# Optimization experiments

Measured on AMD Instinct MI355X. Metric: run time of the kernel, lower is better.

Reference implementation:

```python
import jax, jax.numpy as jnp
import numpy as np

N, IN, HID, OUT, HD = 512, 256, 256, 256, 64  # n_agents, in_dim, hid_dim, out_dim, head_dim (out_dim // n_heads)


def _mlp2(x, w1, b1, w2, b2):
    return jax.nn.relu(x @ w1.T + b1) @ w2.T + b2


def setup_inputs():
    key = jax.random.key(0)
    ks = jax.random.split(key, 32)
    p = lambda i, shape: jax.random.normal(ks[i], shape, dtype=jnp.float32) * 0.05
    V = jax.random.normal(ks[0], (N, IN), dtype=jnp.float32)
    adj = jax.random.randint(ks[1], (N, N), 0, 2, dtype=jnp.int32)
    adj = adj.at[jnp.arange(N), jnp.arange(N)].set(1)  # self-loops so no softmax row is all -inf
    prev_hidden = jax.random.normal(ks[2], (N, HID), dtype=jnp.float32)
    return {
        "V": V, "adj": adj, "prev_hidden": prev_hidden,
        "W1": p(3, (HID, IN)), "sa0": p(4, (HID,)), "sa1": p(5, (HID,)),
        "ce_w1": p(6, (HID, 2 * IN)), "ce_b1": p(7, (HID,)), "ce_w2": p(8, (HD, HID)), "ce_b2": p(9, (HD,)),
        "ca0": p(10, (HD,)), "ca1": p(11, (HD,)),
        "te_w1": p(12, (HID, IN + HID)), "te_b1": p(13, (HID,)), "te_w2": p(14, (HD, HID)), "te_b2": p(15, (HD,)),
        "ta0": p(16, (HD,)), "ta1": p(17, (HD,)),
        "pe_w1": p(18, (HID, 3 * IN)), "pe_b1": p(19, (HID,)), "pe_w2": p(20, (HD, HID)), "pe_b2": p(21, (HD,)),
        "pa0": p(22, (HD,)), "pa1": p(23, (HD,)),
        "W2": p(24, (OUT, HID + 2 * HD + 1)), "op_w": p(25, (OUT, OUT)), "op_b": p(26, (OUT,)),
        "ln_g": jnp.ones((OUT,), jnp.float32), "ln_b": jnp.zeros((OUT,), jnp.float32),
    }


def _forward(V, adj, prev_hidden, W1, sa0, sa1, ce_w1, ce_b1, ce_w2, ce_b2, ca0, ca1,
             te_w1, te_b1, te_w2, te_b2, ta0, ta1, pe_w1, pe_b1, pe_w2, pe_b2, pa0, pa1,
             W2, op_w, op_b, ln_g, ln_b):
    neg = -jnp.inf
    # --- branch 1: standard GAT attention ---
    Wh1 = V @ W1.T                                             # (N, HID)
    s1 = (Wh1 @ sa0)[:, None] + (Wh1 @ sa1)[None, :]           # (N, N)
    s1 = jnp.where(adj == 0, neg, s1)
    H1 = jax.nn.softmax(s1, axis=1) @ Wh1                      # (N, HID)
    # --- branch 2: causal, all ordered pairs i != j ---
    wA, wB = ce_w1[:, :IN], ce_w1[:, IN:]
    h = jax.nn.relu((V @ wA.T)[:, None, :] + (V @ wB.T)[None, :, :] + ce_b1)  # (N, N, HID)
    f = h @ ce_w2.T + ce_b2                                    # (N, N, HD)
    s2 = jnp.where(jnp.eye(N, dtype=bool), neg, f @ (ca0 + ca1))
    a2 = jax.nn.softmax(s2.reshape(-1)).reshape(N, N)          # softmax over all off-diagonal pairs
    H2 = jnp.broadcast_to(jnp.einsum('ij,ijd->d', a2, f), (N, HD))
    # --- branch 3: temporal; (N,1) scores broadcast against (N,N) causal mask ---
    tf = _mlp2(jnp.concatenate([V, prev_hidden], -1), te_w1, te_b1, te_w2, te_b2)  # (N, HD)
    ts = tf @ (ta0 + ta1)                                      # (N,)
    cmask = jnp.triu(jnp.ones((N, N), dtype=bool), 1)
    s3 = jnp.where(cmask, neg, jnp.broadcast_to(ts[:, None], (N, N)))
    H3 = jax.nn.softmax(s3, axis=1) @ tf                       # (N, HD) == prefix means of tf
    # --- branch 4: cooperative; first two neighbors in index order (zeros if < 2) ---
    pos = jnp.where(adj == 1, jnp.arange(N)[None, :], N)
    srt = jnp.sort(pos, axis=1)
    i0, i1 = srt[:, 0], srt[:, 1]
    valid = (i1 < N)[:, None]
    n0 = jnp.where(valid, V[jnp.clip(i0, 0, N - 1)], 0.0)
    n1 = jnp.where(valid, V[jnp.clip(i1, 0, N - 1)], 0.0)
    cf = _mlp2(jnp.concatenate([V, n0, n1], -1), pe_w1, pe_b1, pe_w2, pe_b2)  # (N, HD)
    # torch: softmax over dim of size 1 -> all ones, alpha^T @ cf == column sums -> (HD,)
    # then unsqueezed to (HD,1) and zero-padded to (N,1) since HD < N  (faithful to source bug)
    H4v = cf.sum(axis=0)
    H4 = jnp.concatenate([H4v, jnp.zeros((N - HD,), V.dtype)])[:, None]       # (N, 1)
    # --- combine ---
    Hc = jnp.concatenate([H1, H2, H3, H4], axis=-1) @ W2.T     # (N, OUT)
    out = Hc @ op_w.T + op_b
    mu = out.mean(-1, keepdims=True)
    var = ((out - mu) ** 2).mean(-1, keepdims=True)
    y = (out - mu) / jnp.sqrt(var + 1e-5) * ln_g + ln_b        # LayerNorm, eps=1e-5
    return jax.nn.elu(y)                                       # dropout is identity in eval


def reference(V, adj, prev_hidden, W1, sa0, sa1, ce_w1, ce_b1, ce_w2, ce_b2, ca0, ca1,
              te_w1, te_b1, te_w2, te_b2, ta0, ta1, pe_w1, pe_b1, pe_w2, pe_b2, pa0, pa1,
              W2, op_w, op_b, ln_g, ln_b):
    return _forward(V, adj, prev_hidden, W1, sa0, sa1, ce_w1, ce_b1, ce_w2, ce_b2, ca0, ca1,
                    te_w1, te_b1, te_w2, te_b2, ta0, ta1, pe_w1, pe_b1, pe_w2, pe_b2, pa0, pa1,
                    W2, op_w, op_b, ln_g, ln_b)
```

## Files before the change

### kernel.cpp

```cpp
#include <hip/hip_runtime.h>

typedef unsigned short u16;

constexpr int kN   = 512;
constexpr int kIN  = 256;
constexpr int kHID = 256;
constexpr int kHD  = 64;
constexpr int kOUT = 256;

__device__ __forceinline__ float us2f(u16 u){
  union { unsigned int i; float f; } c; c.i = ((unsigned int)u) << 16; return c.f;
}
__device__ __forceinline__ u16 f2us(float f){
  union { float f; unsigned int i; } c; c.f = f;
  unsigned int r = c.i + 0x7fff + ((c.i >> 16) & 1);
  return (u16)(r >> 16);
}
__device__ __forceinline__ float ldraw(const void* p, size_t i, bool f32){
  return f32 ? ((const float*)p)[i] : us2f(((const u16*)p)[i]);
}

__device__ bool probe_is_f32(const unsigned int* __restrict__ V){
  __shared__ int cnt;
  if (threadIdx.x == 0) cnt = 0;
  __syncthreads();
  int c = 0;
  for (int k = threadIdx.x; k < 4096; k += 256){
    float x = us2f((u16)(V[k] & 0xffffu));
    if (!(fabsf(x) <= 32.0f)) c++;
  }
  atomicAdd(&cnt, c);
  __syncthreads();
  return cnt > 64;
}

__device__ __forceinline__ float blk_red(float v, float* tmp, bool isMax){
  int lane = threadIdx.x & 63, wv = threadIdx.x >> 6;
  #pragma unroll
  for (int o = 32; o > 0; o >>= 1){
    float t = __shfl_down(v, o, 64);
    v = isMax ? fmaxf(v, t) : (v + t);
  }
  __syncthreads();
  if (lane == 0) tmp[wv] = v;
  __syncthreads();
  float r = tmp[0];
  for (int i = 1; i < 4; ++i) r = isMax ? fmaxf(r, tmp[i]) : (r + tmp[i]);
  return r;
}

constexpr int kNConv = 23;
struct ConvArgs { const void* src[kNConv]; float* dst[kNConv]; int n[kNConv]; };
struct GSeg2 { const float* X; const float* W; float* C; int ldx, ldw, ldc, K; };
struct GS32 { const float* X; const float* W; float* C; int ldx, ldw, ldc, K; int bkn; };

struct Args {
  const unsigned int* Vraw;
  const int* adj;
  int* flag; void* out;
  const void *rca0,*rca1,*rcw2,*rcb2,*rtw2,*rpw2;
  float *Vf,*prevf,*W1f,*sa1f,*cw1f,*cb1f,*cw2f,*cb2f,*ca0f,*ca1f;
  float *tw1f,*tb1f,*tw2f,*tb2f,*pw1f,*pb1f,*pw2f,*pb2f;
  float *W2f,*opwf,*opbf,*lngf,*lnbf;
  float *tw2t,*pw2t,*Wcomb,*OM,*ow4;
  float *Wh1,*e1v,*wadj,*Hc,*Am,*Bm,*uvec,*beta;
  float *s2,*maxp,*zp,*MZ,*gsum;
  float *htp0,*htp1,*hpp0,*hpp1,*hpp2,*hidden_t,*hidden_p;
  float *tfm,*cfm,*H4v,*Xp,*out3;
  ConvArgs ca;
  GSeg2 gs[8];
};

__device__ __forceinline__ void gemm32_body(const GS32 sg, int tm, int tn, int tid,
                                            float* Xs, float* Ws)
{
  const int i0 = tm << 5, n0 = tn << 5;
  const int xrow = tid >> 3;
  const int xk = (tid & 7) << 2;
  const int rg = (tid >> 4) << 1;
  const int cg = (tid & 15) << 1;
  const float* Xb = sg.X + (size_t)i0 * sg.ldx;
  const float* Wb = sg.bkn ? (sg.W + n0) : (sg.W + (size_t)n0 * sg.ldw);
  float4 xr, wr;
  auto loadT = [&](int kt){
    xr = *(const float4*)(Xb + (size_t)xrow * sg.ldx + kt + xk);
    if (sg.bkn) wr = *(const float4*)(Wb + (size_t)(kt + xrow) * sg.ldw + xk);
    else        wr = *(const float4*)(Wb + (size_t)xrow * sg.ldw + kt + xk);
  };
  auto writeT = [&](int bu){
    float* xs = Xs + bu*1152;
    xs[(xk+0)*36 + xrow] = xr.x; xs[(xk+1)*36 + xrow] = xr.y;
    xs[(xk+2)*36 + xrow] = xr.z; xs[(xk+3)*36 + xrow] = xr.w;
    float* wsp = Ws + bu*1152;
    if (sg.bkn){
      wsp[xrow*36 + xk+0] = wr.x; wsp[xrow*36 + xk+1] = wr.y;
      wsp[xrow*36 + xk+2] = wr.z; wsp[xrow*36 + xk+3] = wr.w;
    } else {
      wsp[(xk+0)*36 + xrow] = wr.x; wsp[(xk+1)*36 + xrow] = wr.y;
      wsp[(xk+2)*36 + xrow] = wr.z; wsp[(xk+3)*36 + xrow] = wr.w;
    }
  };
  loadT(0); writeT(0); __syncthreads();
  float a00=0,a01=0,a10=0,a11=0;
  const int nkt = sg.K >> 5;
  for (int t = 0; t < nkt; ++t){
    if (t+1 < nkt) loadT((t+1) << 5);
    const float* xs = Xs + (t&1)*1152;
    const float* wsp = Ws + (t&1)*1152;
    #pragma unroll
    for (int kk = 0; kk < 32; ++kk){
      float2 av = *(const float2*)&xs[kk*36 + rg];
      float2 bv = *(const float2*)&wsp[kk*36 + cg];
      a00 += av.x*bv.x; a01 += av.x*bv.y;
      a10 += av.y*bv.x; a11 += av.y*bv.y;
    }
    if (t+1 < nkt) writeT((t+1)&1);
    __syncthreads();
  }
  float* cp = sg.C + (size_t)(i0+rg)*sg.ldc + n0 + cg;
  *(float2*)cp = make_float2(a00, a01);
  *(float2*)(cp + sg.ldc) = make_float2(a10, a11);
}

__device__ void body_gemmA(const Args& A, int it, int tid, char* SM)
{
  float (*Xs)[32][68] = (float (*)[32][68])SM;
  float (*Ws)[32][68] = (float (*)[32][68])(SM + 17408);
  int seg = it >> 5, x = it & 31;
  const GSeg2 sg = A.gs[seg];
  const int tm = x & 7, tn = x >> 3;
  const int i0 = tm << 6, n0 = tn << 6;

  const int xrow = tid >> 3;
  const int xk   = (tid & 7) << 2;
  const int rg = (tid >> 4) << 2;
  const int cg = (tid & 15) << 2;

  const float* Xb = sg.X + (size_t)i0 * sg.ldx;
  const float* Wb = sg.W + (size_t)n0 * sg.ldw;

  float4 xr0, xr1, wr0, wr1;
  auto loadT = [&](int kt){
    xr0 = *(const float4*)(Xb + (size_t)xrow * sg.ldx + kt + xk);
    xr1 = *(const float4*)(Xb + (size_t)(xrow+32) * sg.ldx + kt + xk);
    wr0 = *(const float4*)(Wb + (size_t)xrow * sg.ldw + kt + xk);
    wr1 = *(const float4*)(Wb + (size_t)(xrow+32) * sg.ldw + kt + xk);
  };
  auto writeT = [&](int bu){
    Xs[bu][xk+0][xrow] = xr0.x;  Xs[bu][xk+1][xrow] = xr0.y;
    Xs[bu][xk+2][xrow] = xr0.z;  Xs[bu][xk+3][xrow] = xr0.w;
    Xs[bu][xk+0][xrow+32] = xr1.x;  Xs[bu][xk+1][xrow+32] = xr1.y;
    Xs[bu][xk+2][xrow+32] = xr1.z;  Xs[bu][xk+3][xrow+32] = xr1.w;
    Ws[bu][xk+0][xrow]    = wr0.x; Ws[bu][xk+1][xrow]    = wr0.y;
    Ws[bu][xk+2][xrow]    = wr0.z; Ws[bu][xk+3][xrow]    = wr0.w;
    Ws[bu][xk+0][xrow+32] = wr1.x; Ws[bu][xk+1][xrow+32] = wr1.y;
    Ws[bu][xk+2][xrow+32] = wr1.z; Ws[bu][xk+3][xrow+32] = wr1.w;
  };

  loadT(0); writeT(0); __syncthreads();

  float acc[4][4] = {};
  const int nkt = sg.K >> 5;
  for (int t = 0; t < nkt; ++t){
    if (t + 1 < nkt) loadT((t + 1) << 5);
    const int bu = t & 1;
    #pragma unroll
    for (int kk = 0; kk < 32; ++kk){
      const float4 av = *(const float4*)&Xs[bu][kk][rg];
      const float4 bv = *(const float4*)&Ws[bu][kk][cg];
      acc[0][0]+=av.x*bv.x; acc[0][1]+=av.x*bv.y; acc[0][2]+=av.x*bv.z; acc[0][3]+=av.x*bv.w;
      acc[1][0]+=av.y*bv.x; acc[1][1]+=av.y*bv.y; acc[1][2]+=av.y*bv.z; acc[1][3]+=av.y*bv.w;
      acc[2][0]+=av.z*bv.x; acc[2][1]+=av.z*bv.y; acc[2][2]+=av.z*bv.z; acc[2][3]+=av.z*bv.w;
      acc[3][0]+=av.w*bv.x; acc[3][1]+=av.w*bv.y; acc[3][2]+=av.w*bv.z; acc[3][3]+=av.w*bv.w;
    }
    if (t + 1 < nkt) writeT((t + 1) & 1);
    __syncthreads();
  }

  #pragma unroll
  for (int ri = 0; ri < 4; ++ri)
    *(float4*)(sg.C + (size_t)(i0 + rg + ri) * sg.ldc + (n0 + cg)) =
      make_float4(acc[ri][0], acc[ri][1], acc[ri][2], acc[ri][3]);

  if (seg == 0){
    int cb = n0 + cg;
    float s0 = A.sa1f[cb], s1 = A.sa1f[cb+1], s2v = A.sa1f[cb+2], s3 = A.sa1f[cb+3];
    #pragma unroll
    for (int ri = 0; ri < 4; ++ri){
      float v = acc[ri][0]*s0 + acc[ri][1]*s1 + acc[ri][2]*s2v + acc[ri][3]*s3;
      v += __shfl_xor(v, 1, 16);
      v += __shfl_xor(v, 2, 16);
      v += __shfl_xor(v, 4, 16);
      v += __shfl_xor(v, 8, 16);
      if ((tid & 15) == 0) atomicAdd(&A.e1v[i0 + rg + ri], v);
    }
  }
}

__global__ __launch_bounds__(256) void k_s0(Args A)
{
  __shared__ __align__(16) char SM[16896];
  int it = blockIdx.x, tid = threadIdx.x;
  bool f32 = probe_is_f32(A.Vraw);
  if (it < 256){
    if (it == 0){
      if (tid == 0) *A.flag = f32 ? 1 : 0;
      A.e1v[tid] = 0.f; A.e1v[tid + 256] = 0.f;
    }
    int t = it*256 + tid;
    for (int s = 0; s < kNConv; ++s){
      int n4 = A.ca.n[s] >> 2;
      float4* d = (float4*)A.ca.dst[s];
      if (f32){
        const float4* sf = (const float4*)A.ca.src[s];
        for (int i = t; i < n4; i += 65536) d[i] = sf[i];
      } else {
        const ushort4* sb = (const ushort4*)A.ca.src[s];
        for (int i = t; i < n4; i += 65536){
          ushort4 u = sb[i];
          d[i] = make_float4(us2f(u.x), us2f(u.y), us2f(u.z), us2f(u.w));
        }
      }
    }
  } else if (it < 768){
    unsigned long long* msk = (unsigned long long*)SM;
    int* sj = (int*)(SM + 64);
    int i = it - 256;
    int w = tid >> 6, lane = tid & 63;
    unsigned long long m0 = __ballot(A.adj[(size_t)i*kN + tid] != 0);
    unsigned long long m1 = __ballot(A.adj[(size_t)i*kN + 256 + tid] != 0);
    if (lane == 0){ msk[w] = m0; msk[4 + w] = m1; }
    __syncthreads();
    if (tid == 0){
      int j0 = -1, j1 = -1;
      for (int c = 0; c < 8 && j1 < 0; ++c){
        unsigned long long m = msk[c];
        while (m && j1 < 0){
          int bb = __builtin_ctzll(m);
          int j = c*64 + bb;
          if (j0 < 0) j0 = j; else j1 = j;
          m &= m - 1;
        }
      }
      if (j1 < 0) j0 = -1;
      sj[0] = j0; sj[1] = j1;
    }
    __syncthreads();
    int j0 = sj[0], j1 = sj[1];
    A.Xp[(size_t)i*768 + tid]       = ldraw(A.Vraw, (size_t)i*kIN + tid, f32);
    A.Xp[(size_t)i*768 + 256 + tid] = (j0 >= 0) ? ldraw(A.Vraw, (size_t)j0*kIN + tid, f32) : 0.f;
    A.Xp[(size_t)i*768 + 512 + tid] = (j1 >= 0) ? ldraw(A.Vraw, (size_t)j1*kIN + tid, f32) : 0.f;
  } else if (it == 768){
    float* st = (float*)SM;
    if (tid < 64){ st[tid] = ldraw(A.rca0, tid, f32) + ldraw(A.rca1, tid, f32); A.H4v[tid] = 0.f; }
    __syncthreads();
    float a = 0.f;
    for (int d = 0; d < kHD; ++d) a += ldraw(A.rcw2, (size_t)d*kHID + tid, f32) * st[d];
    A.uvec[tid] = a;
    if (tid == 0){
      float b = 0.f;
      for (int d = 0; d < kHD; ++d) b += ldraw(A.rcb2, d, f32) * st[d];
      *A.beta = b;
    }
  } else {
    const void* src = (it == 769) ? A.rtw2 : A.rpw2;
    float* dst = (it == 769) ? A.tw2t : A.pw2t;
    float* st = (float*)SM;
    for (int ch = 0; ch < 4; ++ch){
      __syncthreads();
      #pragma unroll
      for (int e = 0; e < 16; ++e){
        int lin = e*256 + tid, r = lin >> 6, c = lin & 63;
        st[r*65 + c] = ldraw(src, (size_t)r*256 + ch*64 + c, f32);
      }
      __syncthreads();
      #pragma unroll
      for (int e = 0; e < 16; ++e){
        int lin = e*256 + tid, kc = lin >> 6, dd = lin & 63;
        dst[(size_t)(ch*64 + kc)*64 + dd] = st[dd*65 + kc];
      }
    }
  }
}

__global__ __launch_bounds__(256) void k_s1(Args A)
{
  __shared__ __align__(16) char SM[34816];
  int it = blockIdx.x, tid = threadIdx.x;
  if (it < 256){
    body_gemmA(A, it, tid, SM);
  } else if (it < 336){
    int q = it - 256, tm = q & 7, tn = q >> 3;
    const float* Wsrc = A.W2f + ((tn < 8) ? 0 : 64);
    GS32 sg{A.opwf, Wsrc, A.Wcomb, 256, 385, 320, 256, 1};
    gemm32_body(sg, tm, tn, tid, (float*)SM, (float*)(SM + 9216));
  } else if (it < 352){
    int q = it - 336;
    GS32 sg{A.opwf, A.W2f + 256, A.OM, 256, 385, 64, 256, 1};
    gemm32_body(sg, q & 7, q >> 3, tid, (float*)SM, (float*)(SM + 9216));
  } else {
    float* st = (float*)SM;
    st[tid] = A.W2f[(size_t)tid*385 + 384];
    __syncthreads();
    float a = 0.f;
    const float* orow = A.opwf + (size_t)tid*256;
    for (int m = 0; m < 256; m += 4){
      float4 o4 = *(const float4*)(orow + m);
      a += o4.x*st[m] + o4.y*st[m+1] + o4.z*st[m+2] + o4.w*st[m+3];
    }
    A.ow4[tid] = a;
  }
}

__global__ __launch_bounds__(256) void k_s2(Args A)
{
  __shared__ float SM2[8];
  int it = blockIdx.x, tid = threadIdx.x;
  if (it < 128){
    int f = it*256 + tid;
    int c4 = f & 63;
    {
      float4 a = ((const float4*)A.htp0)[f], bb = ((const float4*)A.htp1)[f];
      float4 bi = ((const float4*)A.tb1f)[c4];
      ((float4*)A.hidden_t)[f] = make_float4(
        fmaxf(a.x+bb.x+bi.x,0.f), fmaxf(a.y+bb.y+bi.y,0.f),
        fmaxf(a.z+bb.z+bi.z,0.f), fmaxf(a.w+bb.w+bi.w,0.f));
    }
    {
      float4 a = ((const float4*)A.hpp0)[f], bb = ((const float4*)A.hpp1)[f];
      float4 c = ((const float4*)A.hpp2)[f];
      float4 bi = ((const float4*)A.pb1f)[c4];
      ((float4*)A.hidden_p)[f] = make_float4(
        fmaxf(a.x+bb.x+c.x+bi.x,0.f), fmaxf(a.y+bb.y+c.y+bi.y,0.f),
        fmaxf(a.z+bb.z+c.z+bi.z,0.f), fmaxf(a.w+bb.w+c.w+bi.w,0.f));
    }
  } else {
    int i = it - 128;
    int m0 = A.adj[(size_t)i*kN + tid];
    int m1 = A.adj[(size_t)i*kN + tid + 256];
    float ea = A.e1v[tid], eb = A.e1v[tid+256];
    float v0 = m0 ? ea : -1e30f;
    float v1 = m1 ? eb : -1e30f;
    float m = blk_red(fmaxf(v0, v1), SM2, true);
    float z = blk_red((m0 ? expf(ea-m) : 0.f) + (m1 ? expf(eb-m) : 0.f), SM2, false);
    float iz = 1.0f / z;
    A.wadj[(size_t)i*kN + tid]       = m0 ? expf(ea - m) * iz : 0.f;
    A.wadj[(size_t)i*kN + tid + 256] = m1 ? expf(eb - m) * iz : 0.f;
  }
}

__global__ __launch_bounds__(256) void k_s3(Args A)
{
  __shared__ __align__(16) float SM3[32*36*2 + 256 + 256 + 8];
  int it = blockIdx.x, tid = threadIdx.x;
  if (it < 64){
    int m = it >> 5, grp = it & 31;
    const float* X  = m ? A.hidden_p : A.hidden_t;
    const float* Wt = m ? A.pw2t : A.tw2t;
    const float* bi = m ? A.pb2f : A.tb2f;
    float* C = m ? A.cfm : A.tfm;
    int i0 = grp*16 + (tid >> 6)*4;
    int d = tid & 63;
    const float* x0 = X + (size_t)i0*256;
    const float* x1 = x0 + 256;
    const float* x2 = x0 + 512;
    const float* x3 = x0 + 768;
    float a0=0.f, a1=0.f, a2=0.f, a3=0.f;
    for (int k = 0; k < 256; k += 4){
      float w0 = Wt[(size_t)(k+0)*64 + d];
      float w1 = Wt[(size_t)(k+1)*64 + d];
      float w2 = Wt[(size_t)(k+2)*64 + d];
      float w3 = Wt[(size_t)(k+3)*64 + d];
      float4 f0 = *(const float4*)(x0 + k);
      float4 f1 = *(const float4*)(x1 + k);
      float4 f2 = *(const float4*)(x2 + k);
      float4 f3 = *(const float4*)(x3 + k);
      a0 += f0.x*w0 + f0.y*w1 + f0.z*w2 + f0.w*w3;
      a1 += f1.x*w0 + f1.y*w1 + f1.z*w2 + f1.w*w3;
      a2 += f2.x*w0 + f2.y*w1 + f2.z*w2 + f2.w*w3;
      a3 += f3.x*w0 + f3.y*w1 + f3.z*w2 + f3.w*w3;
    }
    float bd = bi[d];
    C[(size_t)(i0+0)*64 + d] = a0 + bd;
    C[(size_t)(i0+1)*64 + d] = a1 + bd;
    C[(size_t)(i0+2)*64 + d] = a2 + bd;
    C[(size_t)(i0+3)*64 + d] = a3 + bd;
  } else {
    float* As = SM3;
    float* Bs = As + 32*36;
    float* Us = Bs + 32*36;
    float* B1 = Us + 256;
    float* red = B1 + 256;
    int q = it - 64;
    int i0 = (q & 15) * 32, j0 = (q >> 4) * 32;
    Us[tid] = A.uvec[tid];
    B1[tid] = A.cb1f[tid];
    const int xrow = tid >> 3;
    const int xk   = (tid & 7) << 2;
    const int rg = (tid >> 4) << 1;
    const int cg = (tid & 15) << 1;
    float acc[2][2] = {};
    for (int kt = 0; kt < 256; kt += 32){
      __syncthreads();
      float4 av = *(const float4*)(A.Am + (size_t)(i0+xrow)*kHID + kt + xk);
      float4 bv = *(const float4*)(A.Bm + (size_t)(j0+xrow)*kHID + kt + xk);
      As[(xk+0)*36 + xrow] = av.x + B1[kt+xk+0];
      As[(xk+1)*36 + xrow] = av.y + B1[kt+xk+1];
      As[(xk+2)*36 + xrow] = av.z + B1[kt+xk+2];
      As[(xk+3)*36 + xrow] = av.w + B1[kt+xk+3];
      Bs[(xk+0)*36 + xrow] = bv.x;
      Bs[(xk+1)*36 + xrow] = bv.y;
      Bs[(xk+2)*36 + xrow] = bv.z;
      Bs[(xk+3)*36 + xrow] = bv.w;
      __syncthreads();
      #pragma unroll
      for (int kk = 0; kk < 32; ++kk){
        float uk = Us[kt + kk];
        float2 a2 = *(const float2*)&As[kk*36 + rg];
        float2 b2 = *(const float2*)&Bs[kk*36 + cg];
        acc[0][0] += fmaxf(a2.x + b2.x, 0.f) * uk;
        acc[0][1] += fmaxf(a2.x + b2.y, 0.f) * uk;
        acc[1][0] += fmaxf(a2.y + b2.x, 0.f) * uk;
        acc[1][1] += fmaxf(a2.y + b2.y, 0.f) * uk;
      }
    }
    float bet = *A.beta;
    float sv[2][2];
    #pragma unroll
    for (int r = 0; r < 2; ++r){
      #pragma unroll
      for (int c = 0; c < 2; ++c){
        float vsc = acc[r][c] + bet;
        int i = i0 + rg + r, j = j0 + cg + c;
        if (i == j) vsc = -1e30f;
        sv[r][c] = vsc;
        A.s2[(size_t)i*kN + j] = vsc;
      }
    }
    __syncthreads();
    float m = blk_red(fmaxf(fmaxf(sv[0][0], sv[0][1]), fmaxf(sv[1][0], sv[1][1])), red, true);
    float z = expf(sv[0][0]-m) + expf(sv[0][1]-m) + expf(sv[1][0]-m) + expf(sv[1][1]-m);
    z = blk_red(z, red, false);
    if (tid == 0){ A.maxp[q] = m; A.zp[q] = z; }
  }
}

__global__ __launch_bounds__(256) void k_s4(Args A)
{
  __shared__ __align__(16) char SM[18432];
  int it = blockIdx.x, tid = threadIdx.x;
  if (it < 128){
    GS32 sg{A.wadj, A.Wh1, A.Hc, 512, 256, 320, 512, 1};
    gemm32_body(sg, it & 15, it >> 4, tid, (float*)SM, (float*)(SM + 9216));
  } else if (it < 192){
    int d = it - 128;
    int lane = tid & 63, wv = tid >> 6;
    float v0 = A.tfm[(size_t)(2*tid)*kHD + d];
    float v1 = A.tfm[(size_t)(2*tid+1)*kHD + d];
    float s = v0 + v1;
    float x = s;
    #pragma unroll
    for (int off = 1; off < 64; off <<= 1){
      float y = __shfl_up(x, off, 64);
      if (lane >= off) x += y;
    }
    float* wsum = (float*)SM;
    if (lane == 63) wsum[wv] = x;
    __syncthreads();
    float base = 0.f;
    for (int k = 0; k < wv; ++k) base += wsum[k];
    float excl = base + x - s;
    A.Hc[(size_t)(2*tid)*320 + 256 + d]   = (excl + v0) / (float)(2*tid + 1);
    A.Hc[(size_t)(2*tid+1)*320 + 256 + d] = (excl + s)  / (float)(2*tid + 2);
  } else if (it < 200){
    float* sm = (float*)SM;
    int d = tid & 63, sub = tid >> 6;
    int r0 = (it-192)*64 + sub*16;
    float s = 0.f;
    #pragma unroll
    for (int e = 0; e < 16; ++e) s += A.cfm[(size_t)(r0+e)*kHD + d];
    sm[sub*64 + d] = s;
    __syncthreads();
    if (tid < 64)
      atomicAdd(&A.H4v[tid], sm[tid] + sm[64+tid] + sm[128+tid] + sm[192+tid]);
  } else {
    float* red = (float*)SM;
    float m = blk_red(A.maxp[tid], red, true);
    float z = A.zp[tid] * expf(A.maxp[tid] - m);
    z = blk_red(z, red, false);
    if (tid == 0){ A.MZ[0] = m; A.MZ[1] = z; }
    A.gsum[tid] = 0.f;
  }
}

__global__ __launch_bounds__(256) void k_s5(Args A)
{
  __shared__ __align__(16) char SM[18432];
  int it = blockIdx.x, tid = threadIdx.x;
  if (it < 1024){
    float* wt = (float*)SM;
    int i0 = (it & 31) * 16, j0 = (it >> 5) * 16;
    float M = A.MZ[0], invZ = 1.0f / A.MZ[1];
    {
      int r = tid >> 4, c = tid & 15;
      wt[r*16 + c] = expf(A.s2[(size_t)(i0+r)*kN + (j0+c)] - M) * invZ;
    }
    float b1v = A.cb1f[tid];
    float aib[16];
    #pragma unroll
    for (int r = 0; r < 16; ++r) aib[r] = A.Am[(size_t)(i0+r)*kHID + tid] + b1v;
    __syncthreads();
    float acc = 0.f;
    for (int j = 0; j < 16; ++j){
      float bj = A.Bm[(size_t)(j0+j)*kHID + tid];
      #pragma unroll
      for (int r = 0; r < 16; ++r)
        acc += wt[r*16 + j] * fmaxf(aib[r] + bj, 0.f);
    }
    atomicAdd(&A.gsum[tid], acc);
  } else {
    int q = it - 1024;
    GS32 sg{A.Hc, A.Wcomb, A.out3, 320, 320, 256, 320, 0};
    gemm32_body(sg, q & 15, q >> 4, tid, (float*)SM, (float*)(SM + 9216));
  }
}

__global__ __launch_bounds__(256) void k_s6(Args A)
{
  __shared__ float gs[kHID];
  __shared__ float part[kHD][4];
  __shared__ float h2s[kHD];
  __shared__ float cc2s[kOUT];
  int b = blockIdx.x, tid = threadIdx.x;
  bool f32 = (*A.flag != 0);
  gs[tid] = A.gsum[tid];
  __syncthreads();
  {
    int dd = tid >> 2, q = tid & 3;
    float a = 0.f;
    for (int kk = 0; kk < 64; ++kk){
      int k = q*64 + kk;
      a += gs[k] * A.cw2f[(size_t)dd*kHID + k];
    }
    part[dd][q] = a;
  }
  __syncthreads();
  if (tid < kHD)
    h2s[tid] = A.cb2f[tid] + part[tid][0] + part[tid][1] + part[tid][2] + part[tid][3];
  __syncthreads();
  {
    float a = 0.f;
    const float* om = A.OM + (size_t)tid*64;
    for (int d = 0; d < kHD; d += 4){
      float4 o4 = *(const float4*)(om + d);
      a += o4.x*h2s[d] + o4.y*h2s[d+1] + o4.z*h2s[d+2] + o4.w*h2s[d+3];
    }
    cc2s[tid] = a;
  }
  __syncthreads();
  int row = b*4 + (tid >> 6), lane = tid & 63;
  float h4r = (row < kHD) ? A.H4v[row] : 0.f;
  float4 v  = *(const float4*)(A.out3 + (size_t)row*kOUT + lane*4);
  float4 c2 = *(const float4*)(&cc2s[lane*4]);
  float4 o4 = *(const float4*)(A.ow4 + lane*4);
  float4 pb = *(const float4*)(A.opbf + lane*4);
  v.x += c2.x + h4r*o4.x + pb.x;
  v.y += c2.y + h4r*o4.y + pb.y;
  v.z += c2.z + h4r*o4.z + pb.z;
  v.w += c2.w + h4r*o4.w + pb.w;
  float s = v.x + v.y + v.z + v.w;
  #pragma unroll
  for (int o = 32; o > 0; o >>= 1) s += __shfl_xor(s, o, 64);
  float mu = s * (1.0f/kOUT);
  float dx = v.x-mu, dy = v.y-mu, dz = v.z-mu, dw = v.w-mu;
  float ss = dx*dx + dy*dy + dz*dz + dw*dw;
  #pragma unroll
  for (int o = 32; o > 0; o >>= 1) ss += __shfl_xor(ss, o, 64);
  float rs = rsqrtf(ss * (1.0f/kOUT) + 1e-5f);
  float4 g  = *(const float4*)(A.lngf + lane*4);
  float4 be = *(const float4*)(A.lnbf + lane*4);
  float y0 = dx*rs*g.x + be.x, y1 = dy*rs*g.y + be.y;
  float y2 = dz*rs*g.z + be.z, y3 = dw*rs*g.w + be.w;
  y0 = (y0 > 0.f) ? y0 : expm1f(y0);
  y1 = (y1 > 0.f) ? y1 : expm1f(y1);
  y2 = (y2 > 0.f) ? y2 : expm1f(y2);
  y3 = (y3 > 0.f) ? y3 : expm1f(y3);
  if (f32){
    *(float4*)((float*)A.out + (size_t)row*kOUT + lane*4) = make_float4(y0,y1,y2,y3);
  } else {
    ushort4 u; u.x = f2us(y0); u.y = f2us(y1); u.z = f2us(y2); u.w = f2us(y3);
    ((ushort4*)A.out)[(size_t)row*64 + lane] = u;
  }
}

extern "C" void kernel_launch(void* const* d_in, const int* in_sizes, int n_in,
                              void* d_out, int out_size, void* d_ws, size_t ws_size,
                              hipStream_t stream)
{
  const void* V     = d_in[0];
  const int*  adj   = (const int*)d_in[1];
  const void* prev  = d_in[2];
  const void* W1    = d_in[3];
  const void* sa1   = d_in[5];
  const void* ce_w1 = d_in[6];
  const void* ce_b1 = d_in[7];
  const void* ce_w2 = d_in[8];
  const void* ce_b2 = d_in[9];
  const void* ca0   = d_in[10];
  const void* ca1   = d_in[11];
  const void* te_w1 = d_in[12];
  const void* te_b1 = d_in[13];
  const void* te_w2 = d_in[14];
  const void* te_b2 = d_in[15];
  const void* pe_w1 = d_in[18];
  const void* pe_b1 = d_in[19];
  const void* pe_w2 = d_in[20];
  const void* pe_b2 = d_in[21];
  const void* W2    = d_in[24];
  const void* op_w  = d_in[25];
  const void* op_b  = d_in[26];
  const void* ln_g  = d_in[27];
  const void* ln_b  = d_in[28];

  float* ws  = (float*)d_ws;
  int*  flag = (int*)ws;
  float* p   = ws + 16;
  float* Vf   = p; p += 131072;
  float* prevf= p; p += 131072;
  float* W1f  = p; p += 65536;
  float* sa1f = p; p += 256;
  float* cw1f = p; p += 131072;
  float* cb1f = p; p += 256;
  float* cw2f = p; p += 16384;
  float* cb2f = p; p += 64;
  float* ca0f = p; p += 64;
  float* ca1f = p; p += 64;
  float* tw1f = p; p += 131072;
  float* tb1f = p; p += 256;
  float* tw2f = p; p += 16384;
  float* tb2f = p; p += 64;
  float* pw1f = p; p += 196608;
  float* pb1f = p; p += 256;
  float* pw2f = p; p += 16384;
  float* pb2f = p; p += 64;
  float* W2f  = p; p += 98560;
  float* opwf = p; p += 65536;
  float* opbf = p; p += 256;
  float* lngf = p; p += 256;
  float* lnbf = p; p += 256;
  float* tw2t = p; p += 16384;
  float* pw2t = p; p += 16384;
  float* Wcomb= p; p += 81920;
  float* OM   = p; p += 16384;
  float* ow4  = p; p += 256;
  float* Wh1      = p; p += 131072;
  float* e1v      = p; p += 512;
  float* wadj     = p; p += 262144;
  float* Hc       = p; p += 163840;
  float* Am       = p; p += 131072;
  float* Bm       = p; p += 131072;
  float* uvec     = p; p += 256;
  float* beta     = p; p += 16;
  float* s2       = p; p += 262144;
  float* maxp     = p; p += 4096;
  float* zpart    = p; p += 4096;
  float* MZ       = p; p += 16;
  float* gsum     = p; p += 256;
  float* htp0     = p; p += 131072;
  float* htp1     = p; p += 131072;
  float* hpp0     = p; p += 131072;
  float* hpp1     = p; p += 131072;
  float* hpp2     = p; p += 131072;
  float* hidden_t = p; p += 131072;
  float* hidden_p = p; p += 131072;
  float* tfm      = p; p += 32768;
  float* cfm      = p; p += 32768;
  float* H4v      = p; p += 64;
  float* Xp       = p; p += 393216;
  float* out3     = p; p += 131072;

  Args A;
  A.Vraw = (const unsigned int*)V; A.adj = adj;
  A.flag = flag; A.out = d_out;
  A.rca0 = ca0; A.rca1 = ca1; A.rcw2 = ce_w2; A.rcb2 = ce_b2; A.rtw2 = te_w2; A.rpw2 = pe_w2;
  A.Vf=Vf; A.prevf=prevf; A.W1f=W1f; A.sa1f=sa1f; A.cw1f=cw1f; A.cb1f=cb1f;
  A.cw2f=cw2f; A.cb2f=cb2f; A.ca0f=ca0f; A.ca1f=ca1f;
  A.tw1f=tw1f; A.tb1f=tb1f; A.tw2f=tw2f; A.tb2f=tb2f;
  A.pw1f=pw1f; A.pb1f=pb1f; A.pw2f=pw2f; A.pb2f=pb2f;
  A.W2f=W2f; A.opwf=opwf; A.opbf=opbf; A.lngf=lngf; A.lnbf=lnbf;
  A.tw2t=tw2t; A.pw2t=pw2t; A.Wcomb=Wcomb; A.OM=OM; A.ow4=ow4;
  A.Wh1=Wh1; A.e1v=e1v; A.wadj=wadj; A.Hc=Hc;
  A.Am=Am; A.Bm=Bm; A.uvec=uvec; A.beta=beta;
  A.s2=s2; A.maxp=maxp; A.zp=zpart; A.MZ=MZ; A.gsum=gsum;
  A.htp0=htp0; A.htp1=htp1; A.hpp0=hpp0; A.hpp1=hpp1; A.hpp2=hpp2;
  A.hidden_t=hidden_t; A.hidden_p=hidden_p;
  A.tfm=tfm; A.cfm=cfm; A.H4v=H4v; A.Xp=Xp; A.out3=out3;

  {
    const void* srcs[kNConv] = {V, prev, W1, sa1, ce_w1, ce_b1, ce_w2, ce_b2, ca0, ca1,
                                te_w1, te_b1, te_w2, te_b2, pe_w1, pe_b1, pe_w2, pe_b2,
                                W2, op_w, op_b, ln_g, ln_b};
    float* dsts[kNConv] = {Vf, prevf, W1f, sa1f, cw1f, cb1f, cw2f, cb2f, ca0f, ca1f,
                           tw1f, tb1f, tw2f, tb2f, pw1f, pb1f, pw2f, pb2f,
                           W2f, opwf, opbf, lngf, lnbf};
    int ns[kNConv] = {131072, 131072, 65536, 256, 131072, 256, 16384, 64, 64, 64,
                      131072, 256, 16384, 64, 196608, 256, 16384, 64,
                      98560, 65536, 256, 256, 256};
    for (int s = 0; s < kNConv; ++s){ A.ca.src[s] = srcs[s]; A.ca.dst[s] = dsts[s]; A.ca.n[s] = ns[s]; }
  }
  A.gs[0] = {Vf,       W1f,        Wh1,  256, 256, 256, 256};
  A.gs[1] = {Vf,       cw1f,       Am,   256, 512, 256, 256};
  A.gs[2] = {Vf,       cw1f + 256, Bm,   256, 512, 256, 256};
  A.gs[3] = {Vf,       tw1f,       htp0, 256, 512, 256, 256};
  A.gs[4] = {prevf,    tw1f + 256, htp1, 256, 512, 256, 256};
  A.gs[5] = {Xp,       pw1f,       hpp0, 768, 768, 256, 256};
  A.gs[6] = {Xp + 256, pw1f + 256, hpp1, 768, 768, 256, 256};
  A.gs[7] = {Xp + 512, pw1f + 512, hpp2, 768, 768, 256, 256};

  k_s0<<<771,  256, 0, stream>>>(A);
  k_s1<<<353,  256, 0, stream>>>(A);
  k_s2<<<640,  256, 0, stream>>>(A);
  k_s3<<<320,  256, 0, stream>>>(A);
  k_s4<<<201,  256, 0, stream>>>(A);
  k_s5<<<1152, 256, 0, stream>>>(A);
  k_s6<<<128,  256, 0, stream>>>(A);
}
```

Before: 235.5 us.

## Fuse causal softmax-weighted accumulation into score kernel with per-block max rescale

Each 32x32 score tile now computes its local max and exponentials and immediately accumulates the weighted relu hidden sum into a per-block partial vector. A later reduction rescales these partials by exp(local max minus global max) and divides by the global normalizer. This removes the N×N score buffer round trip, the 1024-block atomicAdd pass and one kernel launch. The hidden_t/hidden_p relu+bias elementwise pass is folded into the downstream GEMV loads, and the final GEMM moves into its own kernel. In exchange the score blocks do more per-block work, partial sums are summed in a different order, and the GEMV reads two or three partial buffers instead of one.

```diff
diff --git a/kernel.cpp b/kernel.cpp
--- a/kernel.cpp
+++ b/kernel.cpp
@@ -64,8 +64,8 @@
   float *W2f,*opwf,*opbf,*lngf,*lnbf;
   float *tw2t,*pw2t,*Wcomb,*OM,*ow4;
   float *Wh1,*e1v,*wadj,*Hc,*Am,*Bm,*uvec,*beta;
-  float *s2,*maxp,*zp,*MZ,*gsum;
-  float *htp0,*htp1,*hpp0,*hpp1,*hpp2,*hidden_t,*hidden_p;
+  float *maxp,*zp,*Gb,*gsum;
+  float *htp0,*htp1,*hpp0,*hpp1,*hpp2;
   float *tfm,*cfm,*H4v,*Xp,*out3;
   ConvArgs ca;
   GSeg2 gs[8];
@@ -314,67 +314,43 @@
 
 __global__ __launch_bounds__(256) void k_s2(Args A)
 {
-  __shared__ float SM2[8];
-  int it = blockIdx.x, tid = threadIdx.x;
-  if (it < 128){
-    int f = it*256 + tid;
-    int c4 = f & 63;
-    {
-      float4 a = ((const float4*)A.htp0)[f], bb = ((const float4*)A.htp1)[f];
-      float4 bi = ((const float4*)A.tb1f)[c4];
-      ((float4*)A.hidden_t)[f] = make_float4(
-        fmaxf(a.x+bb.x+bi.x,0.f), fmaxf(a.y+bb.y+bi.y,0.f),
-        fmaxf(a.z+bb.z+bi.z,0.f), fmaxf(a.w+bb.w+bi.w,0.f));
-    }
-    {
-      float4 a = ((const float4*)A.hpp0)[f], bb = ((const float4*)A.hpp1)[f];
-      float4 c = ((const float4*)A.hpp2)[f];
-      float4 bi = ((const float4*)A.pb1f)[c4];
-      ((float4*)A.hidden_p)[f] = make_float4(
-        fmaxf(a.x+bb.x+c.x+bi.x,0.f), fmaxf(a.y+bb.y+c.y+bi.y,0.f),
-        fmaxf(a.z+bb.z+c.z+bi.z,0.f), fmaxf(a.w+bb.w+c.w+bi.w,0.f));
-    }
-  } else {
-    int i = it - 128;
-    int m0 = A.adj[(size_t)i*kN + tid];
-    int m1 = A.adj[(size_t)i*kN + tid + 256];
-    float ea = A.e1v[tid], eb = A.e1v[tid+256];
-    float v0 = m0 ? ea : -1e30f;
-    float v1 = m1 ? eb : -1e30f;
-    float m = blk_red(fmaxf(v0, v1), SM2, true);
-    float z = blk_red((m0 ? expf(ea-m) : 0.f) + (m1 ? expf(eb-m) : 0.f), SM2, false);
-    float iz = 1.0f / z;
-    A.wadj[(size_t)i*kN + tid]       = m0 ? expf(ea - m) * iz : 0.f;
-    A.wadj[(size_t)i*kN + tid + 256] = m1 ? expf(eb - m) * iz : 0.f;
-  }
-}
-
-__global__ __launch_bounds__(256) void k_s3(Args A)
-{
-  __shared__ __align__(16) float SM3[32*36*2 + 256 + 256 + 8];
+  __shared__ __align__(16) float SM3[1152*2 + 256 + 256 + 1024 + 8];
   int it = blockIdx.x, tid = threadIdx.x;
   if (it < 64){
+    float* B1s = SM3;
     int m = it >> 5, grp = it & 31;
-    const float* X  = m ? A.hidden_p : A.hidden_t;
+    const float* P0 = m ? A.hpp0 : A.htp0;
+    const float* P1 = m ? A.hpp1 : A.htp1;
+    const float* P2 = A.hpp2;
     const float* Wt = m ? A.pw2t : A.tw2t;
     const float* bi = m ? A.pb2f : A.tb2f;
     float* C = m ? A.cfm : A.tfm;
+    B1s[tid] = m ? A.pb1f[tid] : A.tb1f[tid];
+    __syncthreads();
     int i0 = grp*16 + (tid >> 6)*4;
     int d = tid & 63;
-    const float* x0 = X + (size_t)i0*256;
-    const float* x1 = x0 + 256;
-    const float* x2 = x0 + 512;
-    const float* x3 = x0 + 768;
+    size_t r0 = (size_t)i0*256, r1 = r0+256, r2 = r0+512, r3 = r0+768;
     float a0=0.f, a1=0.f, a2=0.f, a3=0.f;
     for (int k = 0; k < 256; k += 4){
       float w0 = Wt[(size_t)(k+0)*64 + d];
       float w1 = Wt[(size_t)(k+1)*64 + d];
       float w2 = Wt[(size_t)(k+2)*64 + d];
       float w3 = Wt[(size_t)(k+3)*64 + d];
-      float4 f0 = *(const float4*)(x0 + k);
-      float4 f1 = *(const float4*)(x1 + k);
-      float4 f2 = *(const float4*)(x2 + k);
-      float4 f3 = *(const float4*)(x3 + k);
+      float4 bb = *(const float4*)&B1s[k];
+      auto ldx = [&](size_t ro)->float4{
+        float4 u0 = *(const float4*)(P0 + ro + k);
+        float4 u1 = *(const float4*)(P1 + ro + k);
+        float4 x = make_float4(u0.x+u1.x+bb.x, u0.y+u1.y+bb.y,
+                               u0.z+u1.z+bb.z, u0.w+u1.w+bb.w);
+        if (m){
+          float4 u2 = *(const float4*)(P2 + ro + k);
+          x.x += u2.x; x.y += u2.y; x.z += u2.z; x.w += u2.w;
+        }
+        x.x = fmaxf(x.x,0.f); x.y = fmaxf(x.y,0.f);
+        x.z = fmaxf(x.z,0.f); x.w = fmaxf(x.w,0.f);
+        return x;
+      };
+      float4 f0 = ldx(r0), f1 = ldx(r1), f2 = ldx(r2), f3 = ldx(r3);
       a0 += f0.x*w0 + f0.y*w1 + f0.z*w2 + f0.w*w3;
       a1 += f1.x*w0 + f1.y*w1 + f1.z*w2 + f1.w*w3;
       a2 += f2.x*w0 + f2.y*w1 + f2.z*w2 + f2.w*w3;
@@ -385,12 +361,13 @@
     C[(size_t)(i0+1)*64 + d] = a1 + bd;
     C[(size_t)(i0+2)*64 + d] = a2 + bd;
     C[(size_t)(i0+3)*64 + d] = a3 + bd;
-  } else {
+  } else if (it < 320){
     float* As = SM3;
-    float* Bs = As + 32*36;
-    float* Us = Bs + 32*36;
+    float* Bs = As + 1152;
+    float* Us = Bs + 1152;
     float* B1 = Us + 256;
-    float* red = B1 + 256;
+    float* wt = B1 + 256;
+    float* red = wt + 1024;
     int q = it - 64;
     int i0 = (q & 15) * 32, j0 = (q >> 4) * 32;
     Us[tid] = A.uvec[tid];
@@ -416,36 +393,70 @@
       #pragma unroll
       for (int kk = 0; kk < 32; ++kk){
         float uk = Us[kt + kk];
-        float2 a2 = *(const float2*)&As[kk*36 + rg];
-        float2 b2 = *(const float2*)&Bs[kk*36 + cg];
-        acc[0][0] += fmaxf(a2.x + b2.x, 0.f) * uk;
-        acc[0][1] += fmaxf(a2.x + b2.y, 0.f) * uk;
-        acc[1][0] += fmaxf(a2.y + b2.x, 0.f) * uk;
-        acc[1][1] += fmaxf(a2.y + b2.y, 0.f) * uk;
+        float2 a2v = *(const float2*)&As[kk*36 + rg];
+        float2 b2v = *(const float2*)&Bs[kk*36 + cg];
+        acc[0][0] += fmaxf(a2v.x + b2v.x, 0.f) * uk;
+        acc[0][1] += fmaxf(a2v.x + b2v.y, 0.f) * uk;
+        acc[1][0] += fmaxf(a2v.y + b2v.x, 0.f) * uk;
+        acc[1][1] += fmaxf(a2v.y + b2v.y, 0.f) * uk;
       }
     }
     float bet = *A.beta;
     float sv[2][2];
     #pragma unroll
-    for (int r = 0; r < 2; ++r){
+    for (int r = 0; r < 2; ++r)
       #pragma unroll
       for (int c = 0; c < 2; ++c){
         float vsc = acc[r][c] + bet;
-        int i = i0 + rg + r, j = j0 + cg + c;
-        if (i == j) vsc = -1e30f;
+        if (i0 + rg + r == j0 + cg + c) vsc = -1e30f;
         sv[r][c] = vsc;
-        A.s2[(size_t)i*kN + j] = vsc;
       }
-    }
-    __syncthreads();
-    float m = blk_red(fmaxf(fmaxf(sv[0][0], sv[0][1]), fmaxf(sv[1][0], sv[1][1])), red, true);
-    float z = expf(sv[0][0]-m) + expf(sv[0][1]-m) + expf(sv[1][0]-m) + expf(sv[1][1]-m);
-    z = blk_red(z, red, false);
-    if (tid == 0){ A.maxp[q] = m; A.zp[q] = z; }
-  }
-}
-
-__global__ __launch_bounds__(256) void k_s4(Args A)
+    float mb = blk_red(fmaxf(fmaxf(sv[0][0], sv[0][1]), fmaxf(sv[1][0], sv[1][1])), red, true);
+    float z4 = 0.f;
+    #pragma unroll
+    for (int r = 0; r < 2; ++r)
+      #pragma unroll
+      for (int c = 0; c < 2; ++c){
+        float wv = expf(sv[r][c] - mb);
+        wt[(rg+r)*32 + (cg+c)] = wv;
+        z4 += wv;
+      }
+    float zb = blk_red(z4, red, false);
+    if (tid == 0){ A.maxp[q] = mb; A.zp[q] = zb; }
+    float b1k = B1[tid];
+    float acck = 0.f;
+    #pragma unroll 1
+    for (int half = 0; half < 2; ++half){
+      float aib[16];
+      #pragma unroll
+      for (int r = 0; r < 16; ++r)
+        aib[r] = A.Am[(size_t)(i0 + half*16 + r)*kHID + tid] + b1k;
+      for (int j = 0; j < 32; ++j){
+        float bj = A.Bm[(size_t)(j0+j)*kHID + tid];
+        const float* wr = &wt[half*16*32 + j];
+        #pragma unroll
+        for (int r = 0; r < 16; ++r)
+          acck += wr[r*32] * fmaxf(aib[r] + bj, 0.f);
+      }
+    }
+    A.Gb[(size_t)q*256 + tid] = acck;
+  } else {
+    float* red = SM3;
+    int i = it - 320;
+    int m0 = A.adj[(size_t)i*kN + tid];
+    int m1 = A.adj[(size_t)i*kN + tid + 256];
+    float ea = A.e1v[tid], eb = A.e1v[tid+256];
+    float v0 = m0 ? ea : -1e30f;
+    float v1 = m1 ? eb : -1e30f;
+    float m = blk_red(fmaxf(v0, v1), red, true);
+    float z = blk_red((m0 ? expf(ea-m) : 0.f) + (m1 ? expf(eb-m) : 0.f), red, false);
+    float iz = 1.0f / z;
+    A.wadj[(size_t)i*kN + tid]       = m0 ? expf(ea - m) * iz : 0.f;
+    A.wadj[(size_t)i*kN + tid + 256] = m1 ? expf(eb - m) * iz : 0.f;
+  }
+}
+
+__global__ __launch_bounds__(256) void k_s3(Args A)
 {
   __shared__ __align__(16) char SM[18432];
   int it = blockIdx.x, tid = threadIdx.x;
@@ -485,47 +496,31 @@
       atomicAdd(&A.H4v[tid], sm[tid] + sm[64+tid] + sm[128+tid] + sm[192+tid]);
   } else {
     float* red = (float*)SM;
-    float m = blk_red(A.maxp[tid], red, true);
-    float z = A.zp[tid] * expf(A.maxp[tid] - m);
-    z = blk_red(z, red, false);
-    if (tid == 0){ A.MZ[0] = m; A.MZ[1] = z; }
-    A.gsum[tid] = 0.f;
-  }
+    float* wb  = red + 8;
+    float mv = A.maxp[tid];
+    float M = blk_red(mv, red, true);
+    float z = A.zp[tid] * expf(mv - M);
+    float Z = blk_red(z, red, false);
+    wb[tid] = expf(mv - M);
+    __syncthreads();
+    float invZ = 1.0f / Z;
+    float g = 0.f;
+    #pragma unroll 4
+    for (int b = 0; b < 256; ++b)
+      g += wb[b] * A.Gb[(size_t)b*256 + tid];
+    A.gsum[tid] = g * invZ;
+  }
+}
+
+__global__ __launch_bounds__(256) void k_s4(Args A)
+{
+  __shared__ __align__(16) char SM[18432];
+  GS32 sg{A.Hc, A.Wcomb, A.out3, 320, 320, 256, 320, 0};
+  gemm32_body(sg, blockIdx.x & 15, blockIdx.x >> 4, threadIdx.x,
+              (float*)SM, (float*)(SM + 9216));
 }
 
 __global__ __launch_bounds__(256) void k_s5(Args A)
-{
-  __shared__ __align__(16) char SM[18432];
-  int it = blockIdx.x, tid = threadIdx.x;
-  if (it < 1024){
-    float* wt = (float*)SM;
-    int i0 = (it & 31) * 16, j0 = (it >> 5) * 16;
-    float M = A.MZ[0], invZ = 1.0f / A.MZ[1];
-    {
-      int r = tid >> 4, c = tid & 15;
-      wt[r*16 + c] = expf(A.s2[(size_t)(i0+r)*kN + (j0+c)] - M) * invZ;
-    }
-    float b1v = A.cb1f[tid];
-    float aib[16];
-    #pragma unroll
-    for (int r = 0; r < 16; ++r) aib[r] = A.Am[(size_t)(i0+r)*kHID + tid] + b1v;
-    __syncthreads();
-    float acc = 0.f;
-    for (int j = 0; j < 16; ++j){
-      float bj = A.Bm[(size_t)(j0+j)*kHID + tid];
-      #pragma unroll
-      for (int r = 0; r < 16; ++r)
-        acc += wt[r*16 + j] * fmaxf(aib[r] + bj, 0.f);
-    }
-    atomicAdd(&A.gsum[tid], acc);
-  } else {
-    int q = it - 1024;
-    GS32 sg{A.Hc, A.Wcomb, A.out3, 320, 320, 256, 320, 0};
-    gemm32_body(sg, q & 15, q >> 4, tid, (float*)SM, (float*)(SM + 9216));
-  }
-}
-
-__global__ __launch_bounds__(256) void k_s6(Args A)
 {
   __shared__ float gs[kHID];
   __shared__ float part[kHD][4];
@@ -661,18 +656,15 @@
   float* Bm       = p; p += 131072;
   float* uvec     = p; p += 256;
   float* beta     = p; p += 16;
-  float* s2       = p; p += 262144;
-  float* maxp     = p; p += 4096;
-  float* zpart    = p; p += 4096;
-  float* MZ       = p; p += 16;
+  float* maxp     = p; p += 256;
+  float* zpart    = p; p += 256;
+  float* Gb       = p; p += 65536;
   float* gsum     = p; p += 256;
   float* htp0     = p; p += 131072;
   float* htp1     = p; p += 131072;
   float* hpp0     = p; p += 131072;
   float* hpp1     = p; p += 131072;
   float* hpp2     = p; p += 131072;
-  float* hidden_t = p; p += 131072;
-  float* hidden_p = p; p += 131072;
   float* tfm      = p; p += 32768;
   float* cfm      = p; p += 32768;
   float* H4v      = p; p += 64;
@@ -691,9 +683,8 @@
   A.tw2t=tw2t; A.pw2t=pw2t; A.Wcomb=Wcomb; A.OM=OM; A.ow4=ow4;
   A.Wh1=Wh1; A.e1v=e1v; A.wadj=wadj; A.Hc=Hc;
   A.Am=Am; A.Bm=Bm; A.uvec=uvec; A.beta=beta;
-  A.s2=s2; A.maxp=maxp; A.zp=zpart; A.MZ=MZ; A.gsum=gsum;
+  A.maxp=maxp; A.zp=zpart; A.Gb=Gb; A.gsum=gsum;
   A.htp0=htp0; A.htp1=htp1; A.hpp0=hpp0; A.hpp1=hpp1; A.hpp2=hpp2;
-  A.hidden_t=hidden_t; A.hidden_p=hidden_p;
   A.tfm=tfm; A.cfm=cfm; A.H4v=H4v; A.Xp=Xp; A.out3=out3;
 
   {
@@ -717,11 +708,10 @@
   A.gs[6] = {Xp + 256, pw1f + 256, hpp1, 768, 768, 256, 256};
   A.gs[7] = {Xp + 512, pw1f + 512, hpp2, 768, 768, 256, 256};
 
-  k_s0<<<771,  256, 0, stream>>>(A);
-  k_s1<<<353,  256, 0, stream>>>(A);
-  k_s2<<<640,  256, 0, stream>>>(A);
-  k_s3<<<320,  256, 0, stream>>>(A);
-  k_s4<<<201,  256, 0, stream>>>(A);
-  k_s5<<<1152, 256, 0, stream>>>(A);
-  k_s6<<<128,  256, 0, stream>>>(A);
-}
+  k_s0<<<771, 256, 0, stream>>>(A);
+  k_s1<<<353, 256, 0, stream>>>(A);
+  k_s2<<<832, 256, 0, stream>>>(A);
+  k_s3<<<201, 256, 0, stream>>>(A);
+  k_s4<<<128, 256, 0, stream>>>(A);
+  k_s5<<<128, 256, 0, stream>>>(A);
+}
```

New measurement: 264.7 us. 1.12x slower.
